# Performance work log

Hardware: AMD Instinct MI355X
Metric: run time of the kernel (lower is better)

The kernel has to match this reference:

```python
import jax, jax.numpy as jnp
import numpy as np

N = 50000      # num nodes
E = 800000     # num edges (before self-loops)
IN = 128       # in_channels
H = 8          # heads (layer 1)
C = 32         # hidden_channels per head
OUT = 64       # out_channels


def setup_inputs() -> dict:
    key = jax.random.key(0)
    ks = jax.random.split(key, 9)
    x = jax.random.normal(ks[0], (N, IN), dtype=jnp.float32)
    edge_index = jax.random.randint(ks[1], (2, E), 0, N, dtype=jnp.int64)
    # layer 1 params (heads=H, concat=True)
    W1 = jax.random.normal(ks[2], (IN, H * C), dtype=jnp.float32) / np.float32(np.sqrt(IN))
    a_src1 = jax.random.normal(ks[3], (H, C), dtype=jnp.float32) / np.float32(np.sqrt(C))
    a_dst1 = jax.random.normal(ks[4], (H, C), dtype=jnp.float32) / np.float32(np.sqrt(C))
    b1 = jnp.zeros((H * C,), dtype=jnp.float32)
    # layer 2 params (heads=1, concat=False)
    W2 = jax.random.normal(ks[5], (H * C, OUT), dtype=jnp.float32) / np.float32(np.sqrt(H * C))
    a_src2 = jax.random.normal(ks[6], (1, OUT), dtype=jnp.float32) / np.float32(np.sqrt(OUT))
    a_dst2 = jax.random.normal(ks[7], (1, OUT), dtype=jnp.float32) / np.float32(np.sqrt(OUT))
    b2 = jnp.zeros((OUT,), dtype=jnp.float32)
    return {"x": x, "edge_index": edge_index,
            "W1": W1, "a_src1": a_src1, "a_dst1": a_dst1, "b1": b1,
            "W2": W2, "a_src2": a_src2, "a_dst2": a_dst2, "b2": b2}


def _gat_layer(x, src, dst, W, a_src, a_dst, b, concat):
    # PyG GATConv (eval mode): linear -> per-head attention logits ->
    # LeakyReLU(0.2) -> segment softmax over destination -> scatter-add.
    Hh, Cc = a_src.shape
    h = (x @ W).reshape(x.shape[0], Hh, Cc)          # [N, H, C]
    al = jnp.sum(h * a_src[None], axis=-1)           # [N, H]
    ar = jnp.sum(h * a_dst[None], axis=-1)           # [N, H]
    e = jax.nn.leaky_relu(al[src] + ar[dst], 0.2)    # [E', H]
    m = jax.ops.segment_max(e, dst, num_segments=N)  # per-dst max (self-loops guarantee coverage)
    p = jnp.exp(e - m[dst])
    s = jax.ops.segment_sum(p, dst, num_segments=N)
    alpha = p / (s[dst] + 1e-16)                     # [E', H]
    out = jax.ops.segment_sum(h[src] * alpha[:, :, None], dst, num_segments=N)  # [N, H, C]
    if concat:
        return out.reshape(N, Hh * Cc) + b
    return jnp.mean(out, axis=1) + b


def reference(x, edge_index, W1, a_src1, a_dst1, b1, W2, a_src2, a_dst2, b2):
    loops = jnp.arange(N, dtype=edge_index.dtype)
    src = jnp.concatenate([edge_index[0], loops])    # add_self_loops=True
    dst = jnp.concatenate([edge_index[1], loops])
    h = _gat_layer(x, src, dst, W1, a_src1, a_dst1, b1, True)   # [N, H*C]
    h = jax.nn.elu(h)                                            # dropout inactive in eval
    return _gat_layer(h, src, dst, W2, a_src2, a_dst2, b2, False)  # [N, OUT]
```

## Files before the change

kernel.cpp:

```cpp
#include <hip/hip_runtime.h>
#include <cstdint>

#define N_NODES 50000
#define N_EDGES 800000
#define E_TOT   (N_EDGES + N_NODES)
#define IN_CH   128
#define HEADS   8
#define CCH     32
#define HC      256
#define OUTC    64

typedef unsigned short ushort_t;
typedef __attribute__((ext_vector_type(8))) short bf16x8;
typedef __attribute__((ext_vector_type(8))) unsigned short u16x8;
typedef __attribute__((ext_vector_type(4))) float f32x4;

static __device__ __forceinline__ unsigned short f2bf(float f) {
    unsigned u = __float_as_uint(f);
    u = u + 0x7fffu + ((u >> 16) & 1u);
    return (unsigned short)(u >> 16);
}
static __device__ __forceinline__ float bf2f(unsigned short h) {
    return __uint_as_float((unsigned)h << 16);
}
static __device__ __forceinline__ unsigned pack2(float lo, float hi) {
    return (unsigned)f2bf(lo) | ((unsigned)f2bf(hi) << 16);
}
static __device__ __forceinline__ float lrexp(float v) {
    v = v > 0.f ? v : 0.2f * v;
    return expf(v);
}
static __device__ __forceinline__ bf16x8 cvt8(float4 lo, float4 hi) {
    bf16x8 r;
    r[0] = (short)f2bf(lo.x); r[1] = (short)f2bf(lo.y);
    r[2] = (short)f2bf(lo.z); r[3] = (short)f2bf(lo.w);
    r[4] = (short)f2bf(hi.x); r[5] = (short)f2bf(hi.y);
    r[6] = (short)f2bf(hi.z); r[7] = (short)f2bf(hi.w);
    return r;
}

__global__ __launch_bounds__(256) void hist_kernel(
        const int* __restrict__ ei, int* __restrict__ deg) {
    int e = blockIdx.x * 256 + threadIdx.x;
    if (e >= E_TOT) return;
    int dv = (e < N_EDGES) ? ei[N_EDGES + e] : (e - N_EDGES);
    atomicAdd(&deg[dv], 1);
}

__global__ __launch_bounds__(1024) void scan1_kernel(
        const int* __restrict__ deg, int* __restrict__ inc, int* __restrict__ bsum) {
    __shared__ int sh[1024];
    const int tid = threadIdx.x;
    const int i = blockIdx.x * 1024 + tid;
    sh[tid] = (i < N_NODES) ? deg[i] : 0;
    __syncthreads();
    for (int o = 1; o < 1024; o <<= 1) {
        int t = (tid >= o) ? sh[tid - o] : 0;
        __syncthreads();
        sh[tid] += t;
        __syncthreads();
    }
    if (i < N_NODES) inc[i] = sh[tid];
    if (tid == 1023) bsum[blockIdx.x] = sh[1023];
}

#define NSCAN_BLOCKS ((N_NODES + 1023) / 1024)
__global__ void scan2_kernel(int* __restrict__ bsum) {
    if (threadIdx.x == 0 && blockIdx.x == 0) {
        int acc = 0;
        for (int k = 0; k < NSCAN_BLOCKS; ++k) { int t = bsum[k]; bsum[k] = acc; acc += t; }
    }
}

__global__ __launch_bounds__(256) void finalize_kernel(
        const int* __restrict__ inc, const int* __restrict__ bsum,
        int* __restrict__ rowstart, int* __restrict__ cursor) {
    int i = blockIdx.x * 256 + threadIdx.x;
    if (i >= N_NODES) return;
    int v = inc[i] + bsum[i >> 10];
    rowstart[i + 1] = v;
    if (i + 1 < N_NODES) cursor[i + 1] = v;
    if (i == 0) { rowstart[0] = 0; cursor[0] = 0; }
}

__global__ __launch_bounds__(256) void scatter_kernel(
        const int* __restrict__ ei, int* __restrict__ cursor,
        int* __restrict__ col, int* __restrict__ row) {
    int e = blockIdx.x * 256 + threadIdx.x;
    if (e >= E_TOT) return;
    int sv, dv;
    if (e < N_EDGES) { sv = ei[e]; dv = ei[N_EDGES + e]; }
    else             { sv = dv = e - N_EDGES; }
    int pos = atomicAdd(&cursor[dv], 1);
    col[pos] = sv;
    row[pos] = dv;
}

__global__ __launch_bounds__(256) void repack_w(
        const float* __restrict__ W1, const float* __restrict__ W2,
        ushort_t* __restrict__ W1f, ushort_t* __restrict__ W2f) {
    int t = blockIdx.x * 256 + threadIdx.x;
    if (t < 32768) {
        int j = t & 7, lane = (t >> 3) & 63, f = t >> 9;
        int nt = f >> 2, kk = f & 3;
        int k = kk * 32 + (lane >> 4) * 8 + j;
        int n = (nt >> 1) * 32 + 2 * (lane & 15) + (nt & 1);
        W1f[t] = f2bf(W1[k * HC + n]);
    } else if (t < 32768 + 16384) {
        int u = t - 32768;
        int j = u & 7, lane = (u >> 3) & 63, f = u >> 9;
        int nt = f >> 3, kk = f & 7;
        int k = kk * 32 + (lane >> 4) * 8 + j;
        int n = (nt >> 1) * 32 + 2 * (lane & 15) + (nt & 1);
        W2f[u] = f2bf(W2[k * OUTC + n]);
    }
}

__global__ __launch_bounds__(256) void gemm1_mfma(
        const float* __restrict__ x, const ushort_t* __restrict__ W1f,
        const float* __restrict__ a_src, const float* __restrict__ a_dst,
        ushort_t* __restrict__ h1b, float* __restrict__ al, float* __restrict__ ar) {
    const int lane = threadIdx.x & 63;
    const int wv   = threadIdx.x >> 6;
    const int base = blockIdx.x * 64 + wv * 16;
    if (base >= N_NODES) return;
    const int am = base + (lane & 15);
    const int rm = am < N_NODES ? am : N_NODES - 1;

    bf16x8 a[4];
    const float* xr = &x[(size_t)rm * IN_CH + (lane >> 4) * 8];
    #pragma unroll
    for (int kk = 0; kk < 4; ++kk) {
        float4 lo = *(const float4*)&xr[kk * 32];
        float4 hi = *(const float4*)&xr[kk * 32 + 4];
        a[kk] = cvt8(lo, hi);
    }

    f32x4 acc[16];
    #pragma unroll
    for (int nt = 0; nt < 16; ++nt) acc[nt] = (f32x4){0.f, 0.f, 0.f, 0.f};

    const bf16x8* bp = (const bf16x8*)W1f;
    #pragma unroll
    for (int nt = 0; nt < 16; ++nt) {
        #pragma unroll
        for (int kk = 0; kk < 4; ++kk)
            acc[nt] = __builtin_amdgcn_mfma_f32_16x16x32_bf16(
                a[kk], bp[(nt * 4 + kk) * 64 + lane], acc[nt], 0, 0, 0);
    }

    #pragma unroll
    for (int r = 0; r < 4; ++r) {
        int node = base + (lane >> 4) * 4 + r;
        if (node < N_NODES) {
            unsigned* op = (unsigned*)&h1b[(size_t)node * HC + 2 * (lane & 15)];
            #pragma unroll
            for (int t = 0; t < 8; ++t)
                op[t * 16] = pack2(acc[2 * t][r], acc[2 * t + 1][r]);
        }
    }

    float asv[16], adv[16];
    #pragma unroll
    for (int nt = 0; nt < 16; ++nt) {
        int n = (nt >> 1) * 32 + 2 * (lane & 15) + (nt & 1);
        asv[nt] = a_src[n];
        adv[nt] = a_dst[n];
    }
    #pragma unroll
    for (int h = 0; h < HEADS; ++h) {
        #pragma unroll
        for (int r = 0; r < 4; ++r) {
            float s = acc[2 * h][r] * asv[2 * h] + acc[2 * h + 1][r] * asv[2 * h + 1];
            float d = acc[2 * h][r] * adv[2 * h] + acc[2 * h + 1][r] * adv[2 * h + 1];
            s += __shfl_xor(s, 1, 64); s += __shfl_xor(s, 2, 64);
            s += __shfl_xor(s, 4, 64); s += __shfl_xor(s, 8, 64);
            d += __shfl_xor(d, 1, 64); d += __shfl_xor(d, 2, 64);
            d += __shfl_xor(d, 4, 64); d += __shfl_xor(d, 8, 64);
            int node = base + (lane >> 4) * 4 + r;
            if ((lane & 15) == 0 && node < N_NODES) {
                al[node * HEADS + h] = s;
                ar[node * HEADS + h] = d;
            }
        }
    }
}

__global__ __launch_bounds__(256) void edge_alpha1(
        const int* __restrict__ col, const int* __restrict__ row,
        const float* __restrict__ al, const float* __restrict__ ar,
        unsigned short* __restrict__ expv) {
    int pos = blockIdx.x * 256 + threadIdx.x;
    if (pos >= E_TOT) return;
    int s = col[pos], d = row[pos];
    const float4* As = (const float4*)&al[s * HEADS];
    const float4* Ad = (const float4*)&ar[d * HEADS];
    float4 a0 = As[0], a1 = As[1], r0 = Ad[0], r1 = Ad[1];
    uint4 o;
    o.x = pack2(lrexp(a0.x + r0.x), lrexp(a0.y + r0.y));
    o.y = pack2(lrexp(a0.z + r0.z), lrexp(a0.w + r0.w));
    o.z = pack2(lrexp(a1.x + r1.x), lrexp(a1.y + r1.y));
    o.w = pack2(lrexp(a1.z + r1.z), lrexp(a1.w + r1.w));
    *(uint4*)&expv[(size_t)pos * 8] = o;
}

__global__ __launch_bounds__(256) void aggr1_csr(
        const int* __restrict__ rowstart, const int* __restrict__ col,
        const unsigned short* __restrict__ expv,
        const unsigned short* __restrict__ h1b, const float* __restrict__ b1,
        unsigned short* __restrict__ out1b) {
    const int lane = threadIdx.x & 63;
    const int d = blockIdx.x * 4 + (threadIdx.x >> 6);
    if (d >= N_NODES) return;
    const int beg = rowstart[d], end = rowstart[d + 1];

    float denom = 0.f;
    for (int i = beg * 8 + lane; i < end * 8; i += 64)
        denom += bf2f(expv[i]);
    denom += __shfl_xor(denom, 8, 64);
    denom += __shfl_xor(denom, 16, 64);
    denom += __shfl_xor(denom, 32, 64);

    const int half = lane >> 5;
    const int L    = lane & 31;
    const int hh   = L >> 2;
    const float inv = 1.f / (__shfl(denom, hh, 64) + 1e-16f);

    float acc8[8] = {0.f,0.f,0.f,0.f,0.f,0.f,0.f,0.f};
    int i = beg;
    for (; i + 7 < end; i += 8) {
        int sv[4]; float wv[4];
        #pragma unroll
        for (int q = 0; q < 4; ++q) sv[q] = col[i + 2 * q + half];
        #pragma unroll
        for (int q = 0; q < 4; ++q)
            wv[q] = bf2f(expv[(i + 2 * q + half) * 8 + hh]) * inv;
        #pragma unroll
        for (int q = 0; q < 4; ++q) {
            const u16x8 v = *(const u16x8*)&h1b[(size_t)sv[q] * HC + L * 8];
            #pragma unroll
            for (int j = 0; j < 8; ++j) acc8[j] += wv[q] * bf2f(v[j]);
        }
    }
    for (; i < end; i += 2) {
        const int e = i + half;
        const bool ok = e < end;
        const int s = col[ok ? e : end - 1];
        const float w = ok ? bf2f(expv[e * 8 + hh]) * inv : 0.f;
        const u16x8 v = *(const u16x8*)&h1b[(size_t)s * HC + L * 8];
        #pragma unroll
        for (int j = 0; j < 8; ++j) acc8[j] += w * bf2f(v[j]);
    }
    #pragma unroll
    for (int j = 0; j < 8; ++j) acc8[j] += __shfl_xor(acc8[j], 32, 64);

    if (half == 0) {
        const float4 b0 = *(const float4*)&b1[L * 8];
        const float4 b4 = *(const float4*)&b1[L * 8 + 4];
        float bb[8] = {b0.x, b0.y, b0.z, b0.w, b4.x, b4.y, b4.z, b4.w};
        u16x8 ov;
        #pragma unroll
        for (int j = 0; j < 8; ++j) {
            float v = acc8[j] + bb[j];
            v = v > 0.f ? v : expf(v) - 1.f;
            ov[j] = f2bf(v);
        }
        *(u16x8*)&out1b[(size_t)d * HC + L * 8] = ov;
    }
}

__global__ __launch_bounds__(256) void gemm2_mfma(
        const ushort_t* __restrict__ hinb, const ushort_t* __restrict__ W2f,
        const float* __restrict__ a_src, const float* __restrict__ a_dst,
        ushort_t* __restrict__ h2b, float* __restrict__ al, float* __restrict__ ar) {
    const int lane = threadIdx.x & 63;
    const int wv   = threadIdx.x >> 6;
    const int base = blockIdx.x * 64 + wv * 16;
    if (base >= N_NODES) return;
    const int am = base + (lane & 15);
    const int rm = am < N_NODES ? am : N_NODES - 1;

    bf16x8 a[8];
    const bf16x8* ap = (const bf16x8*)&hinb[(size_t)rm * HC];
    #pragma unroll
    for (int kk = 0; kk < 8; ++kk)
        a[kk] = ap[kk * 4 + (lane >> 4)];

    f32x4 acc[4];
    #pragma unroll
    for (int nt = 0; nt < 4; ++nt) acc[nt] = (f32x4){0.f, 0.f, 0.f, 0.f};

    const bf16x8* bp = (const bf16x8*)W2f;
    #pragma unroll
    for (int nt = 0; nt < 4; ++nt) {
        #pragma unroll
        for (int kk = 0; kk < 8; ++kk)
            acc[nt] = __builtin_amdgcn_mfma_f32_16x16x32_bf16(
                a[kk], bp[(nt * 8 + kk) * 64 + lane], acc[nt], 0, 0, 0);
    }

    #pragma unroll
    for (int r = 0; r < 4; ++r) {
        int node = base + (lane >> 4) * 4 + r;
        if (node < N_NODES) {
            unsigned* op = (unsigned*)&h2b[(size_t)node * OUTC + 2 * (lane & 15)];
            #pragma unroll
            for (int t = 0; t < 2; ++t)
                op[t * 16] = pack2(acc[2 * t][r], acc[2 * t + 1][r]);
        }
    }

    float asv[4], adv[4];
    #pragma unroll
    for (int nt = 0; nt < 4; ++nt) {
        int n = (nt >> 1) * 32 + 2 * (lane & 15) + (nt & 1);
        asv[nt] = a_src[n];
        adv[nt] = a_dst[n];
    }
    #pragma unroll
    for (int r = 0; r < 4; ++r) {
        float s = 0.f, d = 0.f;
        #pragma unroll
        for (int nt = 0; nt < 4; ++nt) {
            s += acc[nt][r] * asv[nt];
            d += acc[nt][r] * adv[nt];
        }
        s += __shfl_xor(s, 1, 64); s += __shfl_xor(s, 2, 64);
        s += __shfl_xor(s, 4, 64); s += __shfl_xor(s, 8, 64);
        d += __shfl_xor(d, 1, 64); d += __shfl_xor(d, 2, 64);
        d += __shfl_xor(d, 4, 64); d += __shfl_xor(d, 8, 64);
        int node = base + (lane >> 4) * 4 + r;
        if ((lane & 15) == 0 && node < N_NODES) { al[node] = s; ar[node] = d; }
    }
}

__global__ __launch_bounds__(256) void edge_alpha2(
        const int* __restrict__ col, const int* __restrict__ row,
        const float* __restrict__ al, const float* __restrict__ ar,
        float* __restrict__ expv) {
    int pos = blockIdx.x * 256 + threadIdx.x;
    if (pos >= E_TOT) return;
    expv[pos] = lrexp(al[col[pos]] + ar[row[pos]]);
}

__global__ __launch_bounds__(256) void aggr2_csr(
        const int* __restrict__ rowstart, const int* __restrict__ col,
        const float* __restrict__ expv,
        const unsigned short* __restrict__ h2b, const float* __restrict__ b2,
        float* __restrict__ out) {
    const int lane = threadIdx.x & 63;
    const int d = blockIdx.x * 4 + (threadIdx.x >> 6);
    if (d >= N_NODES) return;
    const int beg = rowstart[d], end = rowstart[d + 1];

    float denom = 0.f;
    for (int i = beg + lane; i < end; i += 64)
        denom += expv[i];
    #pragma unroll
    for (int o = 1; o < 64; o <<= 1) denom += __shfl_xor(denom, o, 64);
    const float inv = 1.f / (denom + 1e-16f);

    const int g = lane >> 4;
    const int L = lane & 15;

    float4 acc = {0.f, 0.f, 0.f, 0.f};
    int i = beg;
    for (; i + 7 < end; i += 8) {
        const int s0 = col[i + g], s1 = col[i + 4 + g];
        const float w0 = expv[i + g] * inv, w1 = expv[i + 4 + g] * inv;
        const ushort4 v0 = *(const ushort4*)&h2b[(size_t)s0 * OUTC + L * 4];
        const ushort4 v1 = *(const ushort4*)&h2b[(size_t)s1 * OUTC + L * 4];
        acc.x += w0 * bf2f(v0.x) + w1 * bf2f(v1.x);
        acc.y += w0 * bf2f(v0.y) + w1 * bf2f(v1.y);
        acc.z += w0 * bf2f(v0.z) + w1 * bf2f(v1.z);
        acc.w += w0 * bf2f(v0.w) + w1 * bf2f(v1.w);
    }
    for (; i < end; i += 4) {
        const int e = i + g;
        const bool ok = e < end;
        const int s = col[ok ? e : end - 1];
        const float w = ok ? expv[e] * inv : 0.f;
        const ushort4 v = *(const ushort4*)&h2b[(size_t)s * OUTC + L * 4];
        acc.x += w * bf2f(v.x); acc.y += w * bf2f(v.y);
        acc.z += w * bf2f(v.z); acc.w += w * bf2f(v.w);
    }
    #pragma unroll
    for (int o = 16; o < 64; o <<= 1) {
        acc.x += __shfl_xor(acc.x, o, 64);
        acc.y += __shfl_xor(acc.y, o, 64);
        acc.z += __shfl_xor(acc.z, o, 64);
        acc.w += __shfl_xor(acc.w, o, 64);
    }
    if (g == 0) {
        const float4 bb = *(const float4*)&b2[L * 4];
        float4 ov = { acc.x + bb.x, acc.y + bb.y, acc.z + bb.z, acc.w + bb.w };
        *(float4*)&out[(size_t)d * OUTC + L * 4] = ov;
    }
}

extern "C" void kernel_launch(void* const* d_in, const int* in_sizes, int n_in,
                              void* d_out, int out_size, void* d_ws, size_t ws_size,
                              hipStream_t stream) {
    const float* x      = (const float*)d_in[0];
    const int*   ei     = (const int*)  d_in[1];
    const float* W1     = (const float*)d_in[2];
    const float* a_src1 = (const float*)d_in[3];
    const float* a_dst1 = (const float*)d_in[4];
    const float* b1     = (const float*)d_in[5];
    const float* W2     = (const float*)d_in[6];
    const float* a_src2 = (const float*)d_in[7];
    const float* a_dst2 = (const float*)d_in[8];
    const float* b2     = (const float*)d_in[9];
    float* out = (float*)d_out;

    char* p = (char*)d_ws;
    ushort_t* h1b   = (ushort_t*)p; p += (size_t)N_NODES * HC * 2;
    ushort_t* out1b = (ushort_t*)p; p += (size_t)N_NODES * HC * 2;
    ushort_t* h2b   = (ushort_t*)p; p += (size_t)N_NODES * OUTC * 2;
    ushort_t* expv1 = (ushort_t*)p; p += (size_t)E_TOT * 8 * 2;
    float* expv2 = (float*)p; p += (size_t)E_TOT * sizeof(float);
    ushort_t* W1f  = (ushort_t*)p; p += 32768 * 2;
    ushort_t* W2f  = (ushort_t*)p; p += 16384 * 2;
    float* al1  = (float*)p;  p += (size_t)N_NODES * HEADS * sizeof(float);
    float* ar1  = (float*)p;  p += (size_t)N_NODES * HEADS * sizeof(float);
    float* al2  = (float*)p;  p += (size_t)N_NODES * sizeof(float);
    float* ar2  = (float*)p;  p += (size_t)N_NODES * sizeof(float);
    int* deg      = (int*)p;  p += (size_t)N_NODES * sizeof(int);
    int* inc      = (int*)p;  p += (size_t)N_NODES * sizeof(int);
    int* bsum     = (int*)p;  p += (size_t)NSCAN_BLOCKS * sizeof(int);
    int* rowstart = (int*)p;  p += (size_t)(N_NODES + 1) * sizeof(int);
    int* cursor   = (int*)p;  p += (size_t)N_NODES * sizeof(int);
    int* col      = (int*)p;  p += (size_t)E_TOT * sizeof(int);
    int* row      = (int*)p;  p += (size_t)E_TOT * sizeof(int);

    hipMemsetAsync(deg, 0, (size_t)N_NODES * sizeof(int), stream);
    repack_w       <<<192, 256, 0, stream>>>(W1, W2, W1f, W2f);
    hist_kernel    <<<(E_TOT + 255)/256, 256, 0, stream>>>(ei, deg);
    scan1_kernel   <<<NSCAN_BLOCKS, 1024, 0, stream>>>(deg, inc, bsum);
    scan2_kernel   <<<1, 64, 0, stream>>>(bsum);
    finalize_kernel<<<(N_NODES + 255)/256, 256, 0, stream>>>(inc, bsum, rowstart, cursor);
    scatter_kernel <<<(E_TOT + 255)/256, 256, 0, stream>>>(ei, cursor, col, row);

    gemm1_mfma <<<(N_NODES + 63)/64, 256, 0, stream>>>(x, W1f, a_src1, a_dst1, h1b, al1, ar1);
    edge_alpha1<<<(E_TOT + 255)/256, 256, 0, stream>>>(col, row, al1, ar1, expv1);
    aggr1_csr  <<<(N_NODES + 3)/4, 256, 0, stream>>>(rowstart, col, expv1, h1b, b1, out1b);

    gemm2_mfma <<<(N_NODES + 63)/64, 256, 0, stream>>>(out1b, W2f, a_src2, a_dst2, h2b, al2, ar2);
    edge_alpha2<<<(E_TOT + 255)/256, 256, 0, stream>>>(col, row, al2, ar2, expv2);
    aggr2_csr  <<<(N_NODES + 3)/4, 256, 0, stream>>>(rowstart, col, expv2, h2b, b2, out);
}
```

Before: 261.4 us.

## Fuse edge attention computation into CSR aggregation kernels and drop row array

Removes the separate edge_alpha kernels: each aggregation wavefront now computes the LeakyReLU-exp attention logits from al/ar during its denominator pass and caches them in shared memory for the weighted gather, falling back to recomputation when the row is longer than the cap. This drops the expv buffers, the row array written by scatter, and the scan2 launch, whose prefix is now folded into finalize_kernel. The aim is fewer launches and less global traffic. In exchange it adds shared memory per block, which may lower occupancy, plus redundant per-block prefix sums over the block sums.

```diff
diff --git a/kernel.cpp b/kernel.cpp
--- a/kernel.cpp
+++ b/kernel.cpp
@@ -9,6 +9,8 @@
 #define CCH     32
 #define HC      256
 #define OUTC    64
+#define CAP1    256
+#define CAP2    512
 
 typedef unsigned short ushort_t;
 typedef __attribute__((ext_vector_type(8))) short bf16x8;
@@ -65,27 +67,26 @@
 }
 
 #define NSCAN_BLOCKS ((N_NODES + 1023) / 1024)
-__global__ void scan2_kernel(int* __restrict__ bsum) {
-    if (threadIdx.x == 0 && blockIdx.x == 0) {
-        int acc = 0;
-        for (int k = 0; k < NSCAN_BLOCKS; ++k) { int t = bsum[k]; bsum[k] = acc; acc += t; }
-    }
-}
-
 __global__ __launch_bounds__(256) void finalize_kernel(
         const int* __restrict__ inc, const int* __restrict__ bsum,
         int* __restrict__ rowstart, int* __restrict__ cursor) {
+    __shared__ int pref[NSCAN_BLOCKS];
+    if (threadIdx.x == 0) {
+        int acc = 0;
+        #pragma unroll 7
+        for (int k = 0; k < NSCAN_BLOCKS; ++k) { pref[k] = acc; acc += bsum[k]; }
+    }
+    __syncthreads();
     int i = blockIdx.x * 256 + threadIdx.x;
     if (i >= N_NODES) return;
-    int v = inc[i] + bsum[i >> 10];
+    int v = inc[i] + pref[i >> 10];
     rowstart[i + 1] = v;
     if (i + 1 < N_NODES) cursor[i + 1] = v;
     if (i == 0) { rowstart[0] = 0; cursor[0] = 0; }
 }
 
 __global__ __launch_bounds__(256) void scatter_kernel(
-        const int* __restrict__ ei, int* __restrict__ cursor,
-        int* __restrict__ col, int* __restrict__ row) {
+        const int* __restrict__ ei, int* __restrict__ cursor, int* __restrict__ col) {
     int e = blockIdx.x * 256 + threadIdx.x;
     if (e >= E_TOT) return;
     int sv, dv;
@@ -93,7 +94,6 @@
     else             { sv = dv = e - N_EDGES; }
     int pos = atomicAdd(&cursor[dv], 1);
     col[pos] = sv;
-    row[pos] = dv;
 }
 
 __global__ __launch_bounds__(256) void repack_w(
@@ -186,37 +186,33 @@
     }
 }
 
-__global__ __launch_bounds__(256) void edge_alpha1(
-        const int* __restrict__ col, const int* __restrict__ row,
-        const float* __restrict__ al, const float* __restrict__ ar,
-        unsigned short* __restrict__ expv) {
-    int pos = blockIdx.x * 256 + threadIdx.x;
-    if (pos >= E_TOT) return;
-    int s = col[pos], d = row[pos];
-    const float4* As = (const float4*)&al[s * HEADS];
-    const float4* Ad = (const float4*)&ar[d * HEADS];
-    float4 a0 = As[0], a1 = As[1], r0 = Ad[0], r1 = Ad[1];
-    uint4 o;
-    o.x = pack2(lrexp(a0.x + r0.x), lrexp(a0.y + r0.y));
-    o.y = pack2(lrexp(a0.z + r0.z), lrexp(a0.w + r0.w));
-    o.z = pack2(lrexp(a1.x + r1.x), lrexp(a1.y + r1.y));
-    o.w = pack2(lrexp(a1.z + r1.z), lrexp(a1.w + r1.w));
-    *(uint4*)&expv[(size_t)pos * 8] = o;
-}
-
 __global__ __launch_bounds__(256) void aggr1_csr(
         const int* __restrict__ rowstart, const int* __restrict__ col,
-        const unsigned short* __restrict__ expv,
+        const float* __restrict__ al, const float* __restrict__ ar,
         const unsigned short* __restrict__ h1b, const float* __restrict__ b1,
         unsigned short* __restrict__ out1b) {
+    __shared__ float elds[4][CAP1 * 8];
     const int lane = threadIdx.x & 63;
-    const int d = blockIdx.x * 4 + (threadIdx.x >> 6);
+    const int wrow = threadIdx.x >> 6;
+    const int d = blockIdx.x * 4 + wrow;
     if (d >= N_NODES) return;
     const int beg = rowstart[d], end = rowstart[d + 1];
-
+    const int len = end - beg;
+    const bool fits = len <= CAP1;
+
+    const int h8 = lane & 7;
+    const float ar_h8 = ar[d * HEADS + h8];
     float denom = 0.f;
-    for (int i = beg * 8 + lane; i < end * 8; i += 64)
-        denom += bf2f(expv[i]);
+    if (fits) {
+        for (int i = beg + (lane >> 3); i < end; i += 8) {
+            float e = lrexp(al[col[i] * HEADS + h8] + ar_h8);
+            elds[wrow][(i - beg) * 8 + h8] = e;
+            denom += e;
+        }
+    } else {
+        for (int i = beg + (lane >> 3); i < end; i += 8)
+            denom += lrexp(al[col[i] * HEADS + h8] + ar_h8);
+    }
     denom += __shfl_xor(denom, 8, 64);
     denom += __shfl_xor(denom, 16, 64);
     denom += __shfl_xor(denom, 32, 64);
@@ -225,31 +221,44 @@
     const int L    = lane & 31;
     const int hh   = L >> 2;
     const float inv = 1.f / (__shfl(denom, hh, 64) + 1e-16f);
+    const float ar_hh = ar[d * HEADS + hh];
 
     float acc8[8] = {0.f,0.f,0.f,0.f,0.f,0.f,0.f,0.f};
     int i = beg;
-    for (; i + 7 < end; i += 8) {
-        int sv[4]; float wv[4];
-        #pragma unroll
-        for (int q = 0; q < 4; ++q) sv[q] = col[i + 2 * q + half];
-        #pragma unroll
-        for (int q = 0; q < 4; ++q)
-            wv[q] = bf2f(expv[(i + 2 * q + half) * 8 + hh]) * inv;
-        #pragma unroll
-        for (int q = 0; q < 4; ++q) {
-            const u16x8 v = *(const u16x8*)&h1b[(size_t)sv[q] * HC + L * 8];
-            #pragma unroll
-            for (int j = 0; j < 8; ++j) acc8[j] += wv[q] * bf2f(v[j]);
-        }
-    }
-    for (; i < end; i += 2) {
-        const int e = i + half;
-        const bool ok = e < end;
-        const int s = col[ok ? e : end - 1];
-        const float w = ok ? bf2f(expv[e * 8 + hh]) * inv : 0.f;
-        const u16x8 v = *(const u16x8*)&h1b[(size_t)s * HC + L * 8];
-        #pragma unroll
-        for (int j = 0; j < 8; ++j) acc8[j] += w * bf2f(v[j]);
+    if (fits) {
+        for (; i + 7 < end; i += 8) {
+            int sv[4]; float wv[4];
+            #pragma unroll
+            for (int q = 0; q < 4; ++q) sv[q] = col[i + 2 * q + half];
+            #pragma unroll
+            for (int q = 0; q < 4; ++q)
+                wv[q] = elds[wrow][(i + 2 * q + half - beg) * 8 + hh] * inv;
+            #pragma unroll
+            for (int q = 0; q < 4; ++q) {
+                const u16x8 v = *(const u16x8*)&h1b[(size_t)sv[q] * HC + L * 8];
+                #pragma unroll
+                for (int j = 0; j < 8; ++j) acc8[j] += wv[q] * bf2f(v[j]);
+            }
+        }
+        for (; i < end; i += 2) {
+            const int e = i + half;
+            const bool ok = e < end;
+            const int s = col[ok ? e : end - 1];
+            const float w = ok ? elds[wrow][(e - beg) * 8 + hh] * inv : 0.f;
+            const u16x8 v = *(const u16x8*)&h1b[(size_t)s * HC + L * 8];
+            #pragma unroll
+            for (int j = 0; j < 8; ++j) acc8[j] += w * bf2f(v[j]);
+        }
+    } else {
+        for (; i < end; i += 2) {
+            const int e = i + half;
+            const bool ok = e < end;
+            const int s = col[ok ? e : end - 1];
+            const float w = ok ? lrexp(al[s * HEADS + hh] + ar_hh) * inv : 0.f;
+            const u16x8 v = *(const u16x8*)&h1b[(size_t)s * HC + L * 8];
+            #pragma unroll
+            for (int j = 0; j < 8; ++j) acc8[j] += w * bf2f(v[j]);
+        }
     }
     #pragma unroll
     for (int j = 0; j < 8; ++j) acc8[j] += __shfl_xor(acc8[j], 32, 64);
@@ -334,28 +343,32 @@
     }
 }
 
-__global__ __launch_bounds__(256) void edge_alpha2(
-        const int* __restrict__ col, const int* __restrict__ row,
-        const float* __restrict__ al, const float* __restrict__ ar,
-        float* __restrict__ expv) {
-    int pos = blockIdx.x * 256 + threadIdx.x;
-    if (pos >= E_TOT) return;
-    expv[pos] = lrexp(al[col[pos]] + ar[row[pos]]);
-}
-
 __global__ __launch_bounds__(256) void aggr2_csr(
         const int* __restrict__ rowstart, const int* __restrict__ col,
-        const float* __restrict__ expv,
+        const float* __restrict__ al, const float* __restrict__ ar,
         const unsigned short* __restrict__ h2b, const float* __restrict__ b2,
         float* __restrict__ out) {
+    __shared__ float elds[4][CAP2];
     const int lane = threadIdx.x & 63;
-    const int d = blockIdx.x * 4 + (threadIdx.x >> 6);
+    const int wrow = threadIdx.x >> 6;
+    const int d = blockIdx.x * 4 + wrow;
     if (d >= N_NODES) return;
     const int beg = rowstart[d], end = rowstart[d + 1];
+    const int len = end - beg;
+    const bool fits = len <= CAP2;
+    const float ard = ar[d];
 
     float denom = 0.f;
-    for (int i = beg + lane; i < end; i += 64)
-        denom += expv[i];
+    if (fits) {
+        for (int i = beg + lane; i < end; i += 64) {
+            float e = lrexp(al[col[i]] + ard);
+            elds[wrow][i - beg] = e;
+            denom += e;
+        }
+    } else {
+        for (int i = beg + lane; i < end; i += 64)
+            denom += lrexp(al[col[i]] + ard);
+    }
     #pragma unroll
     for (int o = 1; o < 64; o <<= 1) denom += __shfl_xor(denom, o, 64);
     const float inv = 1.f / (denom + 1e-16f);
@@ -365,24 +378,37 @@
 
     float4 acc = {0.f, 0.f, 0.f, 0.f};
     int i = beg;
-    for (; i + 7 < end; i += 8) {
-        const int s0 = col[i + g], s1 = col[i + 4 + g];
-        const float w0 = expv[i + g] * inv, w1 = expv[i + 4 + g] * inv;
-        const ushort4 v0 = *(const ushort4*)&h2b[(size_t)s0 * OUTC + L * 4];
-        const ushort4 v1 = *(const ushort4*)&h2b[(size_t)s1 * OUTC + L * 4];
-        acc.x += w0 * bf2f(v0.x) + w1 * bf2f(v1.x);
-        acc.y += w0 * bf2f(v0.y) + w1 * bf2f(v1.y);
-        acc.z += w0 * bf2f(v0.z) + w1 * bf2f(v1.z);
-        acc.w += w0 * bf2f(v0.w) + w1 * bf2f(v1.w);
-    }
-    for (; i < end; i += 4) {
-        const int e = i + g;
-        const bool ok = e < end;
-        const int s = col[ok ? e : end - 1];
-        const float w = ok ? expv[e] * inv : 0.f;
-        const ushort4 v = *(const ushort4*)&h2b[(size_t)s * OUTC + L * 4];
-        acc.x += w * bf2f(v.x); acc.y += w * bf2f(v.y);
-        acc.z += w * bf2f(v.z); acc.w += w * bf2f(v.w);
+    if (fits) {
+        for (; i + 7 < end; i += 8) {
+            const int s0 = col[i + g], s1 = col[i + 4 + g];
+            const float w0 = elds[wrow][i + g - beg] * inv;
+            const float w1 = elds[wrow][i + 4 + g - beg] * inv;
+            const ushort4 v0 = *(const ushort4*)&h2b[(size_t)s0 * OUTC + L * 4];
+            const ushort4 v1 = *(const ushort4*)&h2b[(size_t)s1 * OUTC + L * 4];
+            acc.x += w0 * bf2f(v0.x) + w1 * bf2f(v1.x);
+            acc.y += w0 * bf2f(v0.y) + w1 * bf2f(v1.y);
+            acc.z += w0 * bf2f(v0.z) + w1 * bf2f(v1.z);
+            acc.w += w0 * bf2f(v0.w) + w1 * bf2f(v1.w);
+        }
+        for (; i < end; i += 4) {
+            const int e = i + g;
+            const bool ok = e < end;
+            const int s = col[ok ? e : end - 1];
+            const float w = ok ? elds[wrow][e - beg] * inv : 0.f;
+            const ushort4 v = *(const ushort4*)&h2b[(size_t)s * OUTC + L * 4];
+            acc.x += w * bf2f(v.x); acc.y += w * bf2f(v.y);
+            acc.z += w * bf2f(v.z); acc.w += w * bf2f(v.w);
+        }
+    } else {
+        for (; i < end; i += 4) {
+            const int e = i + g;
+            const bool ok = e < end;
+            const int s = col[ok ? e : end - 1];
+            const float w = ok ? lrexp(al[s] + ard) * inv : 0.f;
+            const ushort4 v = *(const ushort4*)&h2b[(size_t)s * OUTC + L * 4];
+            acc.x += w * bf2f(v.x); acc.y += w * bf2f(v.y);
+            acc.z += w * bf2f(v.z); acc.w += w * bf2f(v.w);
+        }
     }
     #pragma unroll
     for (int o = 16; o < 64; o <<= 1) {
@@ -417,8 +443,6 @@
     ushort_t* h1b   = (ushort_t*)p; p += (size_t)N_NODES * HC * 2;
     ushort_t* out1b = (ushort_t*)p; p += (size_t)N_NODES * HC * 2;
     ushort_t* h2b   = (ushort_t*)p; p += (size_t)N_NODES * OUTC * 2;
-    ushort_t* expv1 = (ushort_t*)p; p += (size_t)E_TOT * 8 * 2;
-    float* expv2 = (float*)p; p += (size_t)E_TOT * sizeof(float);
     ushort_t* W1f  = (ushort_t*)p; p += 32768 * 2;
     ushort_t* W2f  = (ushort_t*)p; p += 16384 * 2;
     float* al1  = (float*)p;  p += (size_t)N_NODES * HEADS * sizeof(float);
@@ -431,21 +455,17 @@
     int* rowstart = (int*)p;  p += (size_t)(N_NODES + 1) * sizeof(int);
     int* cursor   = (int*)p;  p += (size_t)N_NODES * sizeof(int);
     int* col      = (int*)p;  p += (size_t)E_TOT * sizeof(int);
-    int* row      = (int*)p;  p += (size_t)E_TOT * sizeof(int);
 
     hipMemsetAsync(deg, 0, (size_t)N_NODES * sizeof(int), stream);
     repack_w       <<<192, 256, 0, stream>>>(W1, W2, W1f, W2f);
     hist_kernel    <<<(E_TOT + 255)/256, 256, 0, stream>>>(ei, deg);
     scan1_kernel   <<<NSCAN_BLOCKS, 1024, 0, stream>>>(deg, inc, bsum);
-    scan2_kernel   <<<1, 64, 0, stream>>>(bsum);
     finalize_kernel<<<(N_NODES + 255)/256, 256, 0, stream>>>(inc, bsum, rowstart, cursor);
-    scatter_kernel <<<(E_TOT + 255)/256, 256, 0, stream>>>(ei, cursor, col, row);
+    scatter_kernel <<<(E_TOT + 255)/256, 256, 0, stream>>>(ei, cursor, col);
 
     gemm1_mfma <<<(N_NODES + 63)/64, 256, 0, stream>>>(x, W1f, a_src1, a_dst1, h1b, al1, ar1);
-    edge_alpha1<<<(E_TOT + 255)/256, 256, 0, stream>>>(col, row, al1, ar1, expv1);
-    aggr1_csr  <<<(N_NODES + 3)/4, 256, 0, stream>>>(rowstart, col, expv1, h1b, b1, out1b);
+    aggr1_csr  <<<(N_NODES + 3)/4, 256, 0, stream>>>(rowstart, col, al1, ar1, h1b, b1, out1b);
 
     gemm2_mfma <<<(N_NODES + 63)/64, 256, 0, stream>>>(out1b, W2f, a_src2, a_dst2, h2b, al2, ar2);
-    edge_alpha2<<<(E_TOT + 255)/256, 256, 0, stream>>>(col, row, al2, ar2, expv2);
-    aggr2_csr  <<<(N_NODES + 3)/4, 256, 0, stream>>>(rowstart, col, expv2, h2b, b2, out);
-}
+    aggr2_csr  <<<(N_NODES + 3)/4, 256, 0, stream>>>(rowstart, col, al2, ar2, h2b, b2, out);
+}
```

Result: slower. 279.6 us (+7.0%).
